# Optimization experiments

Measured on AMD Instinct MI355X. Metric: run time of the kernel, lower is better.

Reference implementation:

```python
import jax, jax.numpy as jnp
import numpy as np

B, S, H, R = 64, 2048, 512, 256
NEG = -1.0e9


def setup_inputs() -> dict:
    key = jax.random.key(0)
    ks = jax.random.split(key, 12)
    sc_h = 1.0 / np.sqrt(H)
    sc_r = 1.0 / np.sqrt(R)
    return {
        "sent_h": jax.random.normal(ks[0], (B, S, H), jnp.float32),
        "rel": jax.random.normal(ks[1], (B, R), jnp.float32),
        "pool": jax.random.normal(ks[2], (B, H), jnp.float32),
        "mask": jax.random.randint(ks[3], (B, S), 0, 2, jnp.int32),
        "Wg_w": jax.random.normal(ks[4], (H, H), jnp.float32) * sc_h,
        "Wg_b": jnp.zeros((H,), jnp.float32),
        "Wh_w": jax.random.normal(ks[5], (H, H), jnp.float32) * sc_h,
        "Wh_b": jnp.zeros((H,), jnp.float32),
        "Wr_w": jax.random.normal(ks[6], (H, R), jnp.float32) * sc_r,
        "Wr_b": jnp.zeros((H,), jnp.float32),
        "alpha_w": jax.random.normal(ks[7], (1, H), jnp.float32) * sc_h,
        "alpha_b": jnp.zeros((1,), jnp.float32),
    }


def reference(sent_h, rel, pool, mask, Wg_w, Wg_b, Wh_w, Wh_b, Wr_w, Wr_b, alpha_w, alpha_b):
    # linear projections (torch Linear: x @ W.T + b)
    relation = rel @ Wr_w.T + Wr_b          # [B, H]
    sent = jnp.einsum('bsh,kh->bsk', sent_h, Wh_w) + Wh_b  # [B, S, H]
    global_sen = pool @ Wg_w.T + Wg_b       # [B, H]
    mix = jnp.tanh(relation[:, None, :] + sent + global_sen[:, None, :])  # [B, S, H]
    weight = jnp.einsum('bsh,h->bs', mix, alpha_w[0]) + alpha_b[0]        # [B, S]
    weight = jnp.where(mask == 0, NEG, weight)
    weight_ = jax.nn.softmax(weight, axis=-1)
    att_res = jnp.einsum('bs,bsh->bh', weight_, sent)  # [B, H]
    return (att_res, weight_)
```

## Files before the change

kernel.cpp:

```cpp
#include <hip/hip_runtime.h>
#include <cstdint>
#include <cstddef>

#define B_ 64
#define S_ 2048
#define H_ 512
#define R_ 256
#define M_ (B_ * S_)
#define NEGV (-1.0e9f)

typedef short short8 __attribute__((ext_vector_type(8)));
typedef unsigned short u16x8 __attribute__((ext_vector_type(8)));
typedef float f32x4 __attribute__((ext_vector_type(4)));
typedef unsigned short u16;

__device__ __forceinline__ u16 f2b(float x) {
    union { float f; uint32_t u; } c; c.f = x;
    uint32_t u = c.u;
    uint32_t r = (u + 0x7fffu + ((u >> 16) & 1u)) >> 16;
    return (u16)r;
}
__device__ __forceinline__ float b2f(u16 u) {
    union { uint32_t u; float f; } c; c.u = ((uint32_t)u) << 16;
    return c.f;
}
__device__ __forceinline__ void load_lds16(const void* g, void* l) {
    __builtin_amdgcn_global_load_lds((__attribute__((address_space(1))) void*)g,
                                     (__attribute__((address_space(3))) void*)l,
                                     16, 0, 0);
}

__global__ void k_convert(const float* __restrict__ sent, u16* __restrict__ sentb) {
    const long tstride = 1048576;
    long i0 = (long)blockIdx.x * 256 + threadIdx.x;
    #pragma unroll
    for (int u = 0; u < 8; ++u) {
        long i = i0 + (long)u * tstride;
        float4 v0 = ((const float4*)sent)[2 * i];
        float4 v1 = ((const float4*)sent)[2 * i + 1];
        u16x8 o;
        o[0] = f2b(v0.x); o[1] = f2b(v0.y); o[2] = f2b(v0.z); o[3] = f2b(v0.w);
        o[4] = f2b(v1.x); o[5] = f2b(v1.y); o[6] = f2b(v1.z); o[7] = f2b(v1.w);
        ((u16x8*)sentb)[i] = o;
    }
}

__global__ void k_base(const float* __restrict__ rel, const float* __restrict__ pool,
                       const float* __restrict__ Wg_w, const float* __restrict__ Wg_b,
                       const float* __restrict__ Wh_b,
                       const float* __restrict__ Wr_w, const float* __restrict__ Wr_b,
                       const float* __restrict__ whw, float* __restrict__ base,
                       u16* __restrict__ whwb) {
    int tid = threadIdx.x;
    {
        int gi = blockIdx.x * 256 + tid;
        float4 v = ((const float4*)whw)[gi];
        ushort4 o; o.x = f2b(v.x); o.y = f2b(v.y); o.z = f2b(v.z); o.w = f2b(v.w);
        ((ushort4*)whwb)[gi] = o;
    }
    int b = blockIdx.x >> 2, q = blockIdx.x & 3;
    __shared__ __attribute__((aligned(16))) float srel[R_];
    __shared__ __attribute__((aligned(16))) float spool[H_];
    __shared__ float accs[128];
    srel[tid & 255] = rel[b * R_ + (tid & 255)];
    for (int i = tid; i < H_; i += 256) spool[i] = pool[b * H_ + i];
    __syncthreads();
    int kk = tid & 127, half = tid >> 7;
    int k = q * 128 + kk;
    float acc = 0.f;
    if (half == 0) {
        acc = Wr_b[k] + Wg_b[k] + Wh_b[k];
        const float4* wr = (const float4*)(Wr_w + (size_t)k * R_);
        #pragma unroll 8
        for (int r4 = 0; r4 < R_ / 4; ++r4) {
            float4 w = wr[r4]; float4 x = ((const float4*)srel)[r4];
            acc += w.x * x.x + w.y * x.y + w.z * x.z + w.w * x.w;
        }
        const float4* wg = (const float4*)(Wg_w + (size_t)k * H_);
        #pragma unroll 8
        for (int h4 = 0; h4 < 32; ++h4) {
            float4 w = wg[h4]; float4 x = ((const float4*)spool)[h4];
            acc += w.x * x.x + w.y * x.y + w.z * x.z + w.w * x.w;
        }
    } else {
        const float4* wg = (const float4*)(Wg_w + (size_t)k * H_);
        #pragma unroll 8
        for (int h4 = 32; h4 < 128; ++h4) {
            float4 w = wg[h4]; float4 x = ((const float4*)spool)[h4];
            acc += w.x * x.x + w.y * x.y + w.z * x.z + w.w * x.w;
        }
    }
    if (half) accs[kk] = acc;
    __syncthreads();
    if (!half) base[b * H_ + k] = acc + accs[kk];
}

__launch_bounds__(256)
__global__ void k_gemm(const u16* __restrict__ A,
                       const u16* __restrict__ Bw,
                       const float* __restrict__ base,
                       const float* __restrict__ alpha,
                       float* __restrict__ partial)
{
    const int K = 512;
    int j = blockIdx.x;
    int xcd  = j & 7;
    int slot = j >> 3;
    int nb   = slot & 3;
    int mb   = (slot >> 2) * 8 + xcd;
    int m0 = mb * 128;
    int n0 = nb * 128;
    int b  = m0 >> 11;

    int tid = threadIdx.x;
    int w  = tid >> 6;
    int l  = tid & 63;
    int wm = w & 1, wn = w >> 1;
    int lr = l & 15;
    int lq = l >> 4;

    __shared__ __attribute__((aligned(16))) u16 smA[2][128 * 64];
    __shared__ __attribute__((aligned(16))) u16 smB[2][128 * 64];
    __shared__ float red[2][2][64];

    f32x4 zero = {0.f, 0.f, 0.f, 0.f};
    f32x4 acc[4][4];
    #pragma unroll
    for (int i = 0; i < 4; ++i)
        #pragma unroll
        for (int jj = 0; jj < 4; ++jj) acc[i][jj] = zero;

    auto STAGE = [&](int buf, int kt) {
        int k0 = kt * 64;
        #pragma unroll
        for (int i = 0; i < 4; ++i) {
            int c  = w * 4 + i;
            int mf = c >> 1, kc = c & 1;
            int row = mf * 16 + lr;
            int col = k0 + kc * 32 + lq * 8;
            const u16* ga = A  + (size_t)(m0 + row) * K + col;
            const u16* gb = Bw + (size_t)(n0 + row) * K + col;
            load_lds16(ga, smA[buf] + c * 512);
            load_lds16(gb, smB[buf] + c * 512);
        }
    };

    STAGE(0, 0);
    __syncthreads();

    #pragma unroll
    for (int kt = 0; kt < 8; ++kt) {
        int cur = kt & 1;
        if (kt < 7) STAGE(cur ^ 1, kt + 1);
        __builtin_amdgcn_s_setprio(1);
        #pragma unroll
        for (int kc = 0; kc < 2; ++kc) {
            short8 af[4], bf[4];
            #pragma unroll
            for (int mi = 0; mi < 4; ++mi)
                af[mi] = *(const short8*)(smA[cur] + ((wm * 4 + mi) * 2 + kc) * 512 + l * 8);
            #pragma unroll
            for (int ni = 0; ni < 4; ++ni)
                bf[ni] = *(const short8*)(smB[cur] + ((wn * 4 + ni) * 2 + kc) * 512 + l * 8);
            #pragma unroll
            for (int mi = 0; mi < 4; ++mi)
                #pragma unroll
                for (int ni = 0; ni < 4; ++ni)
                    acc[mi][ni] = __builtin_amdgcn_mfma_f32_16x16x32_bf16(af[mi], bf[ni], acc[mi][ni], 0, 0, 0);
        }
        __builtin_amdgcn_s_setprio(0);
        __syncthreads();
    }

    const float C2 = 2.8853900817779268f;
    float base2[4], a2[4];
    float asum = 0.f;
    #pragma unroll
    for (int ni = 0; ni < 4; ++ni) {
        int n = n0 + wn * 64 + ni * 16 + lr;
        base2[ni] = C2 * base[b * H_ + n];
        float al  = alpha[n];
        a2[ni] = 2.0f * al;
        asum  += al;
    }
    #pragma unroll
    for (int mi = 0; mi < 4; ++mi) {
        #pragma unroll
        for (int r = 0; r < 4; ++r) {
            float s = asum;
            #pragma unroll
            for (int ni = 0; ni < 4; ++ni) {
                float f  = fmaf(acc[mi][ni][r], C2, base2[ni]);
                float e  = __builtin_amdgcn_exp2f(f);
                float rr = __builtin_amdgcn_rcpf(e + 1.0f);
                s = fmaf(-a2[ni], rr, s);
            }
            s += __shfl_xor(s, 1);
            s += __shfl_xor(s, 2);
            s += __shfl_xor(s, 4);
            s += __shfl_xor(s, 8);
            if (lr == 0) red[wm][wn][mi * 16 + lq * 4 + r] = s;
        }
    }
    __syncthreads();
    if (tid < 128) {
        int wmi = tid >> 6, row = tid & 63;
        float sum = red[wmi][0][row] + red[wmi][1][row];
        partial[(size_t)nb * M_ + m0 + wmi * 64 + row] = sum;
    }
}

__global__ void k_softmax(const float* __restrict__ partial, const int* __restrict__ mask,
                          const float* __restrict__ alpha_b, float* __restrict__ wout) {
    int b = blockIdx.x;
    int tid = threadIdx.x;
    __shared__ float sred[8];
    float x[8];
    float ab = alpha_b[0];
    float lmax = -3.0e38f;
    #pragma unroll
    for (int jj = 0; jj < 8; ++jj) {
        int s = tid + jj * 256;
        size_t m = (size_t)b * S_ + s;
        float v = partial[m] + partial[(size_t)M_ + m] + partial[2 * (size_t)M_ + m] + partial[3 * (size_t)M_ + m] + ab;
        if (mask[b * S_ + s] == 0) v = NEGV;
        x[jj] = v;
        lmax = fmaxf(lmax, v);
    }
    #pragma unroll
    for (int off = 1; off < 64; off <<= 1) lmax = fmaxf(lmax, __shfl_xor(lmax, off));
    int wv = tid >> 6, l = tid & 63;
    if (l == 0) sred[wv] = lmax;
    __syncthreads();
    float gmax = fmaxf(fmaxf(sred[0], sred[1]), fmaxf(sred[2], sred[3]));
    float lsum = 0.f;
    #pragma unroll
    for (int jj = 0; jj < 8; ++jj) { x[jj] = __expf(x[jj] - gmax); lsum += x[jj]; }
    #pragma unroll
    for (int off = 1; off < 64; off <<= 1) lsum += __shfl_xor(lsum, off);
    if (l == 0) sred[4 + wv] = lsum;
    __syncthreads();
    float inv = 1.f / (sred[4] + sred[5] + sred[6] + sred[7]);
    #pragma unroll
    for (int jj = 0; jj < 8; ++jj) {
        int s = tid + jj * 256;
        wout[(size_t)b * S_ + s] = x[jj] * inv;
    }
}

__global__ void k_wsum(const u16* __restrict__ sentb, const float* __restrict__ wrow_g,
                       float* __restrict__ t) {
    int b  = blockIdx.x >> 3;
    int hc = blockIdx.x & 7;
    int tid = threadIdx.x;
    __shared__ __attribute__((aligned(16))) float wrow[S_];
    __shared__ float red[64][33];
    ((float4*)wrow)[tid]       = ((const float4*)(wrow_g + (size_t)b * S_))[tid];
    ((float4*)wrow)[tid + 256] = ((const float4*)(wrow_g + (size_t)b * S_))[tid + 256];
    __syncthreads();
    int hi = tid & 7;
    int sg = tid >> 3;
    const u16* bp = sentb + (size_t)b * S_ * H_ + hc * 64 + hi * 8;
    float acc[8] = {0.f, 0.f, 0.f, 0.f, 0.f, 0.f, 0.f, 0.f};
    #pragma unroll 2
    for (int sb = 0; sb < S_; sb += 256) {
        u16x8 v[8];
        #pragma unroll
        for (int u = 0; u < 8; ++u)
            v[u] = *(const u16x8*)(bp + (size_t)(sb + sg + u * 32) * H_);
        #pragma unroll
        for (int u = 0; u < 8; ++u) {
            float wgt = wrow[sb + sg + u * 32];
            #pragma unroll
            for (int e = 0; e < 8; ++e)
                acc[e] = fmaf(wgt, b2f((u16)v[u][e]), acc[e]);
        }
    }
    #pragma unroll
    for (int e = 0; e < 8; ++e) red[hi * 8 + e][sg] = acc[e];
    __syncthreads();
    if (tid < 64) {
        float s = 0.f;
        #pragma unroll
        for (int g = 0; g < 32; ++g) s += red[tid][g];
        t[(size_t)b * H_ + hc * 64 + tid] = s;
    }
}

__global__ void k_att(const float* __restrict__ t, const float* __restrict__ Whw,
                      const float* __restrict__ Whb, float* __restrict__ out) {
    int tid = threadIdx.x;
    int b = blockIdx.x >> 2, q = blockIdx.x & 3;
    __shared__ __attribute__((aligned(16))) float st[H_];
    __shared__ float accs[128];
    for (int i = tid; i < H_; i += 256) st[i] = t[(size_t)b * H_ + i];
    __syncthreads();
    int hh = tid & 127, half = tid >> 7;
    int h = q * 128 + hh;
    const float4* wr = (const float4*)(Whw + (size_t)h * H_) + half * 64;
    const float4* sx = (const float4*)st + half * 64;
    float acc = 0.f;
    #pragma unroll 8
    for (int i = 0; i < 64; ++i) {
        float4 w = wr[i]; float4 x = sx[i];
        acc += w.x * x.x + w.y * x.y + w.z * x.z + w.w * x.w;
    }
    if (half) accs[hh] = acc;
    __syncthreads();
    if (!half) out[(size_t)b * H_ + h] = acc + accs[hh] + Whb[h];
}

extern "C" void kernel_launch(void* const* d_in, const int* in_sizes, int n_in,
                              void* d_out, int out_size, void* d_ws, size_t ws_size,
                              hipStream_t stream) {
    const float* sent_h  = (const float*)d_in[0];
    const float* rel     = (const float*)d_in[1];
    const float* pool    = (const float*)d_in[2];
    const int*   mask    = (const int*)d_in[3];
    const float* Wg_w    = (const float*)d_in[4];
    const float* Wg_b    = (const float*)d_in[5];
    const float* Wh_w    = (const float*)d_in[6];
    const float* Wh_b    = (const float*)d_in[7];
    const float* Wr_w    = (const float*)d_in[8];
    const float* Wr_b    = (const float*)d_in[9];
    const float* alpha_w = (const float*)d_in[10];
    const float* alpha_b = (const float*)d_in[11];
    float* out = (float*)d_out;

    char* ws = (char*)d_ws;
    u16*   sentb   = (u16*)ws;
    u16*   whwb    = (u16*)(ws + 134217728);
    float* base    = (float*)(ws + 134217728 + 524288);
    float* partial = (float*)(ws + 134217728 + 524288 + 131072);
    float* tbuf    = (float*)(ws + 134217728 + 524288 + 131072 + 2097152);

    float* att_out = out;
    float* w_out   = out + B_ * H_;

    k_convert<<<dim3(4096), dim3(256), 0, stream>>>(sent_h, sentb);
    k_base<<<dim3(256), dim3(256), 0, stream>>>(rel, pool, Wg_w, Wg_b, Wh_b, Wr_w, Wr_b, Wh_w, base, whwb);
    k_gemm<<<dim3((M_ / 128) * 4), dim3(256), 0, stream>>>(sentb, whwb, base, alpha_w, partial);
    k_softmax<<<dim3(B_), dim3(256), 0, stream>>>(partial, mask, alpha_b, w_out);
    k_wsum<<<dim3(B_ * 8), dim3(256), 0, stream>>>(sentb, w_out, tbuf);
    k_att<<<dim3(256), dim3(256), 0, stream>>>(tbuf, Wh_w, Wh_b, att_out);
}
```

Before: 590.7 us.

## Fuse fp32-to-bf16 conversion of sent_h into GEMM staging and read fp32 in wsum

Removes the separate conversion kernel that wrote a bf16 copy of the large activation tensor. The GEMM now loads fp32 rows into registers, packs them to bf16 with v_cvt_pk_bf16_f32, and writes them to LDS after the MFMA work of each k-step. The weighted-sum kernel reads fp32 directly instead of the bf16 copy. This cuts a full write plus read pass over the tensor, at the cost of doubled per-read bytes in the GEMM and wsum and more register pressure in the GEMM.

Result: faster. 578.6 us (-2.1%).

```diff
diff --git a/kernel.cpp b/kernel.cpp
--- a/kernel.cpp
+++ b/kernel.cpp
@@ -24,25 +24,15 @@
     union { uint32_t u; float f; } c; c.u = ((uint32_t)u) << 16;
     return c.f;
 }
+__device__ __forceinline__ uint32_t pk2(float lo, float hi) {
+    uint32_t r;
+    asm("v_cvt_pk_bf16_f32 %0, %1, %2" : "=v"(r) : "v"(lo), "v"(hi));
+    return r;
+}
 __device__ __forceinline__ void load_lds16(const void* g, void* l) {
     __builtin_amdgcn_global_load_lds((__attribute__((address_space(1))) void*)g,
                                      (__attribute__((address_space(3))) void*)l,
                                      16, 0, 0);
-}
-
-__global__ void k_convert(const float* __restrict__ sent, u16* __restrict__ sentb) {
-    const long tstride = 1048576;
-    long i0 = (long)blockIdx.x * 256 + threadIdx.x;
-    #pragma unroll
-    for (int u = 0; u < 8; ++u) {
-        long i = i0 + (long)u * tstride;
-        float4 v0 = ((const float4*)sent)[2 * i];
-        float4 v1 = ((const float4*)sent)[2 * i + 1];
-        u16x8 o;
-        o[0] = f2b(v0.x); o[1] = f2b(v0.y); o[2] = f2b(v0.z); o[3] = f2b(v0.w);
-        o[4] = f2b(v1.x); o[5] = f2b(v1.y); o[6] = f2b(v1.z); o[7] = f2b(v1.w);
-        ((u16x8*)sentb)[i] = o;
-    }
 }
 
 __global__ void k_base(const float* __restrict__ rel, const float* __restrict__ pool,
@@ -96,7 +86,7 @@
 }
 
 __launch_bounds__(256)
-__global__ void k_gemm(const u16* __restrict__ A,
+__global__ void k_gemm(const float* __restrict__ A32,
                        const u16* __restrict__ Bw,
                        const float* __restrict__ base,
                        const float* __restrict__ alpha,
@@ -130,7 +120,37 @@
         #pragma unroll
         for (int jj = 0; jj < 4; ++jj) acc[i][jj] = zero;
 
-    auto STAGE = [&](int buf, int kt) {
+    int arow[4], acolg[4];
+    #pragma unroll
+    for (int i = 0; i < 4; ++i) {
+        int c = w * 4 + i;
+        arow[i]  = (c >> 1) * 16 + lr;
+        acolg[i] = (c & 1) * 32 + lq * 8;
+    }
+
+    float4 av[4][2];
+
+    auto LOAD_A = [&](int kt) {
+        int k0 = kt * 64;
+        #pragma unroll
+        for (int i = 0; i < 4; ++i) {
+            const float4* ga = (const float4*)(A32 + (size_t)(m0 + arow[i]) * K + k0 + acolg[i]);
+            av[i][0] = ga[0];
+            av[i][1] = ga[1];
+        }
+    };
+    auto WRITE_A = [&](int buf) {
+        #pragma unroll
+        for (int i = 0; i < 4; ++i) {
+            uint4 pv;
+            pv.x = pk2(av[i][0].x, av[i][0].y);
+            pv.y = pk2(av[i][0].z, av[i][0].w);
+            pv.z = pk2(av[i][1].x, av[i][1].y);
+            pv.w = pk2(av[i][1].z, av[i][1].w);
+            *(uint4*)(smA[buf] + (w * 4 + i) * 512 + l * 8) = pv;
+        }
+    };
+    auto STAGE_B = [&](int buf, int kt) {
         int k0 = kt * 64;
         #pragma unroll
         for (int i = 0; i < 4; ++i) {
@@ -138,20 +158,23 @@
             int mf = c >> 1, kc = c & 1;
             int row = mf * 16 + lr;
             int col = k0 + kc * 32 + lq * 8;
-            const u16* ga = A  + (size_t)(m0 + row) * K + col;
             const u16* gb = Bw + (size_t)(n0 + row) * K + col;
-            load_lds16(ga, smA[buf] + c * 512);
             load_lds16(gb, smB[buf] + c * 512);
         }
     };
 
-    STAGE(0, 0);
+    LOAD_A(0);
+    STAGE_B(0, 0);
+    WRITE_A(0);
     __syncthreads();
 
     #pragma unroll
     for (int kt = 0; kt < 8; ++kt) {
         int cur = kt & 1;
-        if (kt < 7) STAGE(cur ^ 1, kt + 1);
+        if (kt < 7) {
+            LOAD_A(kt + 1);
+            STAGE_B(cur ^ 1, kt + 1);
+        }
         __builtin_amdgcn_s_setprio(1);
         #pragma unroll
         for (int kc = 0; kc < 2; ++kc) {
@@ -169,6 +192,7 @@
                     acc[mi][ni] = __builtin_amdgcn_mfma_f32_16x16x32_bf16(af[mi], bf[ni], acc[mi][ni], 0, 0, 0);
         }
         __builtin_amdgcn_s_setprio(0);
+        if (kt < 7) WRITE_A(cur ^ 1);
         __syncthreads();
     }
 
@@ -248,7 +272,7 @@
     }
 }
 
-__global__ void k_wsum(const u16* __restrict__ sentb, const float* __restrict__ wrow_g,
+__global__ void k_wsum(const float* __restrict__ sent, const float* __restrict__ wrow_g,
                        float* __restrict__ t) {
     int b  = blockIdx.x >> 3;
     int hc = blockIdx.x & 7;
@@ -260,20 +284,26 @@
     __syncthreads();
     int hi = tid & 7;
     int sg = tid >> 3;
-    const u16* bp = sentb + (size_t)b * S_ * H_ + hc * 64 + hi * 8;
+    const float* bp = sent + (size_t)b * S_ * H_ + hc * 64 + hi * 8;
     float acc[8] = {0.f, 0.f, 0.f, 0.f, 0.f, 0.f, 0.f, 0.f};
-    #pragma unroll 2
     for (int sb = 0; sb < S_; sb += 256) {
-        u16x8 v[8];
-        #pragma unroll
-        for (int u = 0; u < 8; ++u)
-            v[u] = *(const u16x8*)(bp + (size_t)(sb + sg + u * 32) * H_);
+        float4 v[8][2];
+        #pragma unroll
+        for (int u = 0; u < 8; ++u) {
+            const float4* p = (const float4*)(bp + (size_t)(sb + sg + u * 32) * H_);
+            v[u][0] = p[0]; v[u][1] = p[1];
+        }
         #pragma unroll
         for (int u = 0; u < 8; ++u) {
             float wgt = wrow[sb + sg + u * 32];
-            #pragma unroll
-            for (int e = 0; e < 8; ++e)
-                acc[e] = fmaf(wgt, b2f((u16)v[u][e]), acc[e]);
+            acc[0] = fmaf(wgt, v[u][0].x, acc[0]);
+            acc[1] = fmaf(wgt, v[u][0].y, acc[1]);
+            acc[2] = fmaf(wgt, v[u][0].z, acc[2]);
+            acc[3] = fmaf(wgt, v[u][0].w, acc[3]);
+            acc[4] = fmaf(wgt, v[u][1].x, acc[4]);
+            acc[5] = fmaf(wgt, v[u][1].y, acc[5]);
+            acc[6] = fmaf(wgt, v[u][1].z, acc[6]);
+            acc[7] = fmaf(wgt, v[u][1].w, acc[7]);
         }
     }
     #pragma unroll
@@ -328,19 +358,17 @@
     float* out = (float*)d_out;
 
     char* ws = (char*)d_ws;
-    u16*   sentb   = (u16*)ws;
-    u16*   whwb    = (u16*)(ws + 134217728);
-    float* base    = (float*)(ws + 134217728 + 524288);
-    float* partial = (float*)(ws + 134217728 + 524288 + 131072);
-    float* tbuf    = (float*)(ws + 134217728 + 524288 + 131072 + 2097152);
+    u16*   whwb    = (u16*)ws;
+    float* base    = (float*)(ws + 524288);
+    float* partial = (float*)(ws + 524288 + 131072);
+    float* tbuf    = (float*)(ws + 524288 + 131072 + 2097152);
 
     float* att_out = out;
     float* w_out   = out + B_ * H_;
 
-    k_convert<<<dim3(4096), dim3(256), 0, stream>>>(sent_h, sentb);
     k_base<<<dim3(256), dim3(256), 0, stream>>>(rel, pool, Wg_w, Wg_b, Wh_b, Wr_w, Wr_b, Wh_w, base, whwb);
-    k_gemm<<<dim3((M_ / 128) * 4), dim3(256), 0, stream>>>(sentb, whwb, base, alpha_w, partial);
+    k_gemm<<<dim3((M_ / 128) * 4), dim3(256), 0, stream>>>(sent_h, whwb, base, alpha_w, partial);
     k_softmax<<<dim3(B_), dim3(256), 0, stream>>>(partial, mask, alpha_b, w_out);
-    k_wsum<<<dim3(B_ * 8), dim3(256), 0, stream>>>(sentb, w_out, tbuf);
+    k_wsum<<<dim3(B_ * 8), dim3(256), 0, stream>>>(sent_h, w_out, tbuf);
     k_att<<<dim3(256), dim3(256), 0, stream>>>(tbuf, Wh_w, Wh_b, att_out);
 }
```
